# Optimization experiments

Measured on AMD Instinct MI355X. Metric: run time of the kernel, lower is better.

Reference implementation:

```python
import jax, jax.numpy as jnp
import numpy as np

BS = 1024
IN_DIM = 16 * 16      # final_dim[0]*final_dim[1]
HIDDEN = 3000
ITEM = 3              # item_number
STEPS = 30


def setup_inputs() -> dict:
    key = jax.random.key(0)
    ks = jax.random.split(key, 16)

    def xavier(k, shape):
        fan_in, fan_out = shape[1], shape[0]
        lim = np.sqrt(6.0 / (fan_in + fan_out))
        return jax.random.uniform(k, shape, jnp.float32, -lim, lim)

    return {
        "z": jax.random.normal(ks[0], (BS, 16, 16), jnp.float32),
        # join MLP: in->512->256->3000, ReLU after each
        "W1": xavier(ks[1], (512, IN_DIM)), "b1": jnp.zeros((512,), jnp.float32),
        "W2": xavier(ks[2], (256, 512)),    "b2": jnp.zeros((256,), jnp.float32),
        "W3": xavier(ks[3], (HIDDEN, 256)), "b3": jnp.zeros((HIDDEN,), jnp.float32),
        # GRUCell (torch layout: rows ordered r, z, n)
        "Wih": xavier(ks[4], (3 * HIDDEN, ITEM)),
        "bih": jnp.zeros((3 * HIDDEN,), jnp.float32),
        "Whh": xavier(ks[5], (3 * HIDDEN, HIDDEN)),
        "bhh": jnp.zeros((3 * HIDDEN,), jnp.float32),
        # output readout hidden -> item_number
        "Wo": xavier(ks[6], (ITEM, HIDDEN)), "bo": jnp.zeros((ITEM,), jnp.float32),
    }


def reference(z, W1, b1, W2, b2, W3, b3, Wih, bih, Whh, bhh, Wo, bo):
    bs = z.shape[0]
    zf = z.reshape(bs, -1)                                  # [bs, 256]
    h = jax.nn.relu(zf @ W1.T + b1)
    h = jax.nn.relu(h @ W2.T + b2)
    h = jax.nn.relu(h @ W3.T + b3)                          # [bs, 3000] initial hidden
    x0 = jnp.zeros((bs, ITEM), z.dtype)

    def step(carry, _):
        h, x = carry
        gi = x @ Wih.T + bih                                # [bs, 3H]
        gh = h @ Whh.T + bhh                                # [bs, 3H]
        i_r, i_z, i_n = jnp.split(gi, 3, axis=-1)
        h_r, h_z, h_n = jnp.split(gh, 3, axis=-1)
        r = jax.nn.sigmoid(i_r + h_r)
        u = jax.nn.sigmoid(i_z + h_z)
        n = jnp.tanh(i_n + r * h_n)
        h_new = (1.0 - u) * n + u * h
        x_new = h_new @ Wo.T + bo + x                       # residual waypoint add
        return (h_new, x_new), x_new

    (_, _), wp = jax.lax.scan(step, (h, x0), None, length=STEPS)
    return jnp.transpose(wp, (1, 0, 2))                      # [bs, STEPS, ITEM]
```

## Files before the change

kernel.cpp:

```cpp
#include <hip/hip_runtime.h>
#include <cstdint>
#include <cstddef>

#define HID 3000
#define HP  3072
#define NB  1024
#define BM  128
#define BN  64
#define KT  48

typedef _Float16 f16;
typedef _Float16 f16x8 __attribute__((ext_vector_type(8)));
typedef float    f32x4 __attribute__((ext_vector_type(4)));

__device__ __forceinline__ float sigf(float v)  { return 1.0f / (1.0f + __expf(-v)); }
__device__ __forceinline__ float tanhf_(float v){ return 2.0f / (1.0f + __expf(-2.0f * v)) - 1.0f; }

__device__ __forceinline__ void gload16(const void* g, void* l) {
    __builtin_amdgcn_global_load_lds((const __attribute__((address_space(1))) void*)g,
                                     (__attribute__((address_space(3))) void*)l, 16, 0, 0);
}

__global__ __launch_bounds__(256) void convert_whh(const float* __restrict__ whh,
                                                   f16* __restrict__ whh16)
{
    const int SLOTS = 3 * HP * (HP / 8);
    int t = blockIdx.x * 256 + threadIdx.x;
    if (t >= SLOTS) return;
    int c8 = (t % (HP / 8)) * 8;
    int rr = (t / (HP / 8)) % HP;
    int g  = t / ((HP / 8) * HP);
    f16x8 v;
#pragma unroll
    for (int i = 0; i < 8; ++i) v[i] = (f16)0.0f;
    if (rr < HID) {
        const float* src = whh + (size_t)(g * HID + rr) * HID;
#pragma unroll
        for (int i = 0; i < 8; ++i) {
            int c = c8 + i;
            if (c < HID) v[i] = (f16)src[c];
        }
    }
    *reinterpret_cast<f16x8*>(whh16 + ((size_t)g * HP + rr) * HP + c8) = v;
}

__global__ __launch_bounds__(256) void convert_w3(const float* __restrict__ w,
                                                  f16* __restrict__ w16)
{
    int t = blockIdx.x * 256 + threadIdx.x;
    if (t >= HP * 32) return;
    int rr = t >> 5, c8 = (t & 31) * 8;
    f16x8 v;
#pragma unroll
    for (int i = 0; i < 8; ++i)
        v[i] = (rr < HID) ? (f16)w[(size_t)rr * 256 + c8 + i] : (f16)0.0f;
    *reinterpret_cast<f16x8*>(w16 + (size_t)rr * 256 + c8) = v;
}

__global__ __launch_bounds__(256) void mlp_layer(const float* __restrict__ A, int K, int N, int ldo,
                                                 const float* __restrict__ W,
                                                 const float* __restrict__ bias,
                                                 float* __restrict__ outf, f16* __restrict__ outh)
{
    __shared__ float sA[4 * 512];
    const int b0 = blockIdx.x * 4;
    for (int idx = threadIdx.x; idx < 4 * K; idx += 256)
        sA[idx] = A[(size_t)b0 * K + idx];
    __syncthreads();
    for (int n = threadIdx.x; n < ldo; n += 256) {
        float acc[4] = {0.f, 0.f, 0.f, 0.f};
        if (n < N) {
            const float4* wr = reinterpret_cast<const float4*>(W + (size_t)n * K);
            for (int kk = 0; kk < (K >> 2); ++kk) {
                float4 w = wr[kk];
#pragma unroll
                for (int r = 0; r < 4; ++r) {
                    const float* ar = sA + r * K + kk * 4;
                    acc[r] += ar[0] * w.x + ar[1] * w.y + ar[2] * w.z + ar[3] * w.w;
                }
            }
            float bv = bias[n];
#pragma unroll
            for (int r = 0; r < 4; ++r) acc[r] = fmaxf(acc[r] + bv, 0.f);
        }
#pragma unroll
        for (int r = 0; r < 4; ++r) {
            outf[(size_t)(b0 + r) * ldo + n] = acc[r];
            if (outh) outh[(size_t)(b0 + r) * ldo + n] = (f16)acc[r];
        }
    }
}

__global__ __launch_bounds__(256, 2)
void mlp3_mfma(const f16* __restrict__ A, const f16* __restrict__ B,
               const float* __restrict__ bias,
               float* __restrict__ outf, f16* __restrict__ outh)
{
    __shared__ __align__(16) char smem[24576];
    char* sBm = smem + 16384;

    const int tid  = threadIdx.x;
    const int lane = tid & 63;
    const int wid  = tid >> 6;
    const int wm = wid >> 1, wn = wid & 1;
    const int l15 = lane & 15, lhi = lane >> 4;
    const int swz = (lane & 7) << 4;

    const int gm0 = blockIdx.y * BM, gn0 = blockIdx.x * BN;

    const f16* a_srcs[4]; char* a_ldst[4];
#pragma unroll
    for (int i = 0; i < 4; ++i) {
        const int d = (i * 4 + wid) * 64 + lane;
        const int r = d >> 3;
        const int c = (d & 7) ^ (r & 7);
        a_srcs[i] = A + (size_t)(gm0 + r) * 256 + c * 8;
        a_ldst[i] = smem + (i * 4 + wid) * 1024;
    }
    const f16* b_srcs[2]; char* b_ldst[2];
#pragma unroll
    for (int i = 0; i < 2; ++i) {
        const int d = (i * 4 + wid) * 64 + lane;
        const int rr = d >> 3;
        const int c = (d & 7) ^ (rr & 7);
        b_srcs[i] = B + (size_t)(gn0 + rr) * 256 + c * 8;
        b_ldst[i] = sBm + (i * 4 + wid) * 1024;
    }

    f32x4 acc[4][2];
#pragma unroll
    for (int m = 0; m < 4; ++m)
#pragma unroll
        for (int n = 0; n < 2; ++n) acc[m][n] = (f32x4){0.f, 0.f, 0.f, 0.f};

    for (int kt = 0; kt < 4; ++kt) {
        const int kg = kt * 64;
#pragma unroll
        for (int i = 0; i < 4; ++i) gload16(a_srcs[i] + kg, a_ldst[i]);
#pragma unroll
        for (int i = 0; i < 2; ++i) gload16(b_srcs[i] + kg, b_ldst[i]);
        __syncthreads();
#pragma unroll
        for (int kk = 0; kk < 2; ++kk) {
            const int ko = (kk * 64 + lhi * 16) ^ swz;
            f16x8 af[4], bf[2];
#pragma unroll
            for (int m = 0; m < 4; ++m)
                af[m] = *reinterpret_cast<const f16x8*>(smem + (wm * 64 + m * 16 + l15) * 128 + ko);
#pragma unroll
            for (int n = 0; n < 2; ++n)
                bf[n] = *reinterpret_cast<const f16x8*>(sBm + (wn * 32 + n * 16 + l15) * 128 + ko);
#pragma unroll
            for (int m = 0; m < 4; ++m)
#pragma unroll
                for (int n = 0; n < 2; ++n)
                    acc[m][n] = __builtin_amdgcn_mfma_f32_16x16x32_f16(af[m], bf[n], acc[m][n], 0, 0, 0);
        }
        __syncthreads();
    }

#pragma unroll
    for (int m = 0; m < 4; ++m) {
#pragma unroll
        for (int e = 0; e < 4; ++e) {
            const int b = gm0 + wm * 64 + m * 16 + lhi * 4 + e;
#pragma unroll
            for (int n = 0; n < 2; ++n) {
                const int j = gn0 + wn * 32 + n * 16 + l15;
                if (j < HID) {
                    float v = fmaxf(acc[m][n][e] + bias[j], 0.f);
                    outf[(size_t)b * HP + j] = v;
                    outh[(size_t)b * HP + j] = (f16)v;
                }
            }
        }
    }
}

__global__ __launch_bounds__(256, 2)
void gru_step(const f16* __restrict__ h16c, float* __restrict__ hf32,
              const f16* __restrict__ whh16,
              const float* __restrict__ xprev,
              const float* __restrict__ Wih, const float* __restrict__ bih,
              const float* __restrict__ bhh,
              f16* __restrict__ h16n)
{
    __shared__ __align__(16) char smem[69632];

    const int tid  = threadIdx.x;
    const int lane = tid & 63;
    const int wid  = tid >> 6;
    const int l15 = lane & 15, lhi = lane >> 4;
    const int swz = (lane & 7) << 4;

    const int id = blockIdx.x;
    const int xcd = id & 7, j0 = id >> 3;
    const int bn = xcd * 8 + (j0 >> 3), bm = j0 & 7;
    const int gm0 = bm * 128, gn0 = bn * 48;

    const f16* a_src[4];
#pragma unroll
    for (int i = 0; i < 4; ++i) {
        const int d = i * 256 + tid;
        const int r = d >> 3;
        const int c = (d & 7) ^ (r & 7);
        a_src[i] = h16c + (size_t)(gm0 + r) * HP + c * 8;
    }
    const f16* b_src[5];
#pragma unroll
    for (int i = 0; i < 5; ++i) {
        const int d = i * 256 + tid;
        const int g = d / 384;
        const int s = d - g * 384;
        const int rr = s >> 3;
        const int c = (s & 7) ^ (rr & 7);
        b_src[i] = whh16 + (size_t)g * HP * HP + (size_t)(gn0 + rr) * HP + c * 8;
    }

    f32x4 acc[3][2][3];
#pragma unroll
    for (int g = 0; g < 3; ++g)
#pragma unroll
        for (int m = 0; m < 2; ++m)
#pragma unroll
            for (int n = 0; n < 3; ++n) acc[g][m][n] = (f32x4){0.f, 0.f, 0.f, 0.f};

    {
#pragma unroll
        for (int i = 0; i < 4; ++i) gload16(a_src[i], smem + i * 4096 + wid * 1024);
#pragma unroll
        for (int i = 0; i < 4; ++i) gload16(b_src[i], smem + 16384 + i * 4096 + wid * 1024);
        if (tid < 128) gload16(b_src[4], smem + 32768 + wid * 1024);
    }
    __syncthreads();

    for (int kt = 0; kt < KT; ++kt) {
        char* cbuf = smem + (kt & 1) * 34816;
        if (kt + 1 < KT) {
            char* nbuf = smem + ((kt + 1) & 1) * 34816;
            const int kg = (kt + 1) * 64;
#pragma unroll
            for (int i = 0; i < 4; ++i) gload16(a_src[i] + kg, nbuf + i * 4096 + wid * 1024);
#pragma unroll
            for (int i = 0; i < 4; ++i) gload16(b_src[i] + kg, nbuf + 16384 + i * 4096 + wid * 1024);
            if (tid < 128) gload16(b_src[4] + kg, nbuf + 32768 + wid * 1024);
        }
#pragma unroll
        for (int kk = 0; kk < 2; ++kk) {
            const int ko = (kk * 64 + lhi * 16) ^ swz;
            f16x8 af[2], bf[3][3];
#pragma unroll
            for (int m = 0; m < 2; ++m)
                af[m] = *reinterpret_cast<const f16x8*>(cbuf + (wid * 32 + m * 16 + l15) * 128 + ko);
#pragma unroll
            for (int g = 0; g < 3; ++g)
#pragma unroll
                for (int n = 0; n < 3; ++n)
                    bf[g][n] = *reinterpret_cast<const f16x8*>(cbuf + 16384 + g * 6144 + (n * 16 + l15) * 128 + ko);
#pragma unroll
            for (int g = 0; g < 3; ++g)
#pragma unroll
                for (int m = 0; m < 2; ++m)
#pragma unroll
                    for (int n = 0; n < 3; ++n)
                        acc[g][m][n] = __builtin_amdgcn_mfma_f32_16x16x32_f16(af[m], bf[g][n], acc[g][m][n], 0, 0, 0);
        }
        __syncthreads();
    }

#pragma unroll
    for (int m = 0; m < 2; ++m) {
#pragma unroll
        for (int e = 0; e < 4; ++e) {
            const int b = gm0 + wid * 32 + m * 16 + lhi * 4 + e;
            const float x0 = xprev[b * 4 + 0], x1 = xprev[b * 4 + 1], x2 = xprev[b * 4 + 2];
#pragma unroll
            for (int n = 0; n < 3; ++n) {
                const int j = gn0 + n * 16 + l15;
                if (j < HID) {
                    float g0 = acc[0][m][n][e];
                    float g1 = acc[1][m][n][e];
                    float g2 = acc[2][m][n][e];
                    const float* wr = Wih + (size_t)j * 3;
                    const float* wz = Wih + (size_t)(HID + j) * 3;
                    const float* wn_ = Wih + (size_t)(2 * HID + j) * 3;
                    float gi0 = x0 * wr[0] + x1 * wr[1] + x2 * wr[2] + bih[j];
                    float gi1 = x0 * wz[0] + x1 * wz[1] + x2 * wz[2] + bih[HID + j];
                    float gi2 = x0 * wn_[0] + x1 * wn_[1] + x2 * wn_[2] + bih[2 * HID + j];
                    float r = sigf(gi0 + g0 + bhh[j]);
                    float u = sigf(gi1 + g1 + bhh[HID + j]);
                    float nn = tanhf_(gi2 + r * (g2 + bhh[2 * HID + j]));
                    float hp_ = hf32[(size_t)b * HP + j];
                    float hn = (1.f - u) * nn + u * hp_;
                    hf32[(size_t)b * HP + j] = hn;
                    h16n[(size_t)b * HP + j] = (f16)hn;
                }
            }
        }
    }
}

__global__ __launch_bounds__(256) void x_update(const f16* __restrict__ hn,
                                                const float* __restrict__ Wo,
                                                const float* __restrict__ bo,
                                                const float* __restrict__ xp,
                                                float* __restrict__ xn,
                                                float* __restrict__ out, int s)
{
    const int b = blockIdx.x, tid = threadIdx.x;
    float a0 = 0.f, a1 = 0.f, a2 = 0.f;
    for (int ch = tid; ch < 375; ch += 256) {
        const int k = ch * 8;
        f16x8 h8 = *reinterpret_cast<const f16x8*>(hn + (size_t)b * HP + k);
#pragma unroll
        for (int i = 0; i < 8; ++i) {
            float hv = (float)h8[i];
            a0 += hv * Wo[k + i];
            a1 += hv * Wo[HID + k + i];
            a2 += hv * Wo[2 * HID + k + i];
        }
    }
#pragma unroll
    for (int off = 32; off; off >>= 1) {
        a0 += __shfl_down(a0, off);
        a1 += __shfl_down(a1, off);
        a2 += __shfl_down(a2, off);
    }
    __shared__ float red[3][4];
    const int lane = tid & 63, w = tid >> 6;
    if (lane == 0) { red[0][w] = a0; red[1][w] = a1; red[2][w] = a2; }
    __syncthreads();
    if (tid < 3) {
        float sres = red[tid][0] + red[tid][1] + red[tid][2] + red[tid][3];
        float xv = sres + bo[tid] + xp[b * 4 + tid];
        xn[b * 4 + tid] = xv;
        out[((size_t)b * 30 + s) * 3 + tid] = xv;
    }
}

extern "C" void kernel_launch(void* const* d_in, const int* in_sizes, int n_in,
                              void* d_out, int out_size, void* d_ws, size_t ws_size,
                              hipStream_t stream)
{
    (void)in_sizes; (void)n_in; (void)out_size; (void)ws_size;
    const float* z   = (const float*)d_in[0];
    const float* W1  = (const float*)d_in[1];
    const float* b1  = (const float*)d_in[2];
    const float* W2  = (const float*)d_in[3];
    const float* b2  = (const float*)d_in[4];
    const float* W3  = (const float*)d_in[5];
    const float* b3  = (const float*)d_in[6];
    const float* Wih = (const float*)d_in[7];
    const float* bih = (const float*)d_in[8];
    const float* Whh = (const float*)d_in[9];
    const float* bhh = (const float*)d_in[10];
    const float* Wo  = (const float*)d_in[11];
    const float* bo  = (const float*)d_in[12];
    float* out = (float*)d_out;

    char* ws = (char*)d_ws;
    size_t off = 0;
    f16* whh16 = (f16*)(ws + off); off += (size_t)3 * HP * HP * 2;
    f16* h16[2];
    h16[0] = (f16*)(ws + off); off += (size_t)NB * HP * 2;
    h16[1] = (f16*)(ws + off); off += (size_t)NB * HP * 2;
    float* hf  = (float*)(ws + off); off += (size_t)NB * HP * 4;
    float* h1  = (float*)(ws + off); off += (size_t)NB * 512 * 4;
    float* h2  = (float*)(ws + off); off += (size_t)NB * 256 * 4;
    f16*   h2h = (f16*)(ws + off);   off += (size_t)NB * 256 * 2;
    f16*   w3f16 = (f16*)(ws + off); off += (size_t)HP * 256 * 2;
    float* xb  = (float*)(ws + off); off += (size_t)31 * NB * 4 * 4;

    hipMemsetAsync(h16[0], 0, (size_t)2 * NB * HP * 2, stream);
    hipMemsetAsync(xb, 0, (size_t)NB * 4 * 4, stream);

    {
        int slots = 3 * HP * (HP / 8);
        convert_whh<<<(slots + 255) / 256, 256, 0, stream>>>(Whh, whh16);
    }
    convert_w3<<<(HP * 32 + 255) / 256, 256, 0, stream>>>(W3, w3f16);

    mlp_layer<<<NB / 4, 256, 0, stream>>>(z,  256, 512, 512, W1, b1, h1, nullptr);
    mlp_layer<<<NB / 4, 256, 0, stream>>>(h1, 512, 256, 256, W2, b2, h2, h2h);
    mlp3_mfma<<<dim3(HP / BN, NB / BM), 256, 0, stream>>>(h2h, w3f16, b3, hf, h16[0]);

    for (int s = 1; s <= 30; ++s) {
        int cur = (s - 1) & 1, nxt = s & 1;
        gru_step<<<512, 256, 0, stream>>>(
            h16[cur], hf, whh16, xb + (size_t)(s - 1) * NB * 4,
            Wih, bih, bhh, h16[nxt]);
        x_update<<<NB, 256, 0, stream>>>(h16[nxt], Wo, bo,
            xb + (size_t)(s - 1) * NB * 4, xb + (size_t)s * NB * 4, out, s - 1);
    }
}
```

Measured before the change: 2.386 ms.

## Split K across warps in GRU step GEMM and vectorize weight conversion

The GRU step kernel now assigns each warp a 64-row M half and one of the two 32-wide K sub-slices per tile, instead of 32 rows over the full K tile. This doubles the MFMAs per A fragment load and cuts per-warp LDS reads of the shared B fragments, at the cost of 72 accumulator registers per lane and a two-pass shared-memory reduction with extra barriers before the epilogue. Only half the warps then run the gate epilogue. The weight conversion kernels also switch to float4 loads, which removes per-element bounds checks.

```diff
diff --git a/kernel.cpp b/kernel.cpp
--- a/kernel.cpp
+++ b/kernel.cpp
@@ -31,15 +31,15 @@
     int rr = (t / (HP / 8)) % HP;
     int g  = t / ((HP / 8) * HP);
     f16x8 v;
-#pragma unroll
-    for (int i = 0; i < 8; ++i) v[i] = (f16)0.0f;
-    if (rr < HID) {
-        const float* src = whh + (size_t)(g * HID + rr) * HID;
-#pragma unroll
-        for (int i = 0; i < 8; ++i) {
-            int c = c8 + i;
-            if (c < HID) v[i] = (f16)src[c];
-        }
+    if (rr < HID && c8 < HID) {
+        const float* src = whh + (size_t)(g * HID + rr) * HID + c8;
+        float4 lo = *reinterpret_cast<const float4*>(src);
+        float4 hi = *reinterpret_cast<const float4*>(src + 4);
+        v[0] = (f16)lo.x; v[1] = (f16)lo.y; v[2] = (f16)lo.z; v[3] = (f16)lo.w;
+        v[4] = (f16)hi.x; v[5] = (f16)hi.y; v[6] = (f16)hi.z; v[7] = (f16)hi.w;
+    } else {
+#pragma unroll
+        for (int i = 0; i < 8; ++i) v[i] = (f16)0.0f;
     }
     *reinterpret_cast<f16x8*>(whh16 + ((size_t)g * HP + rr) * HP + c8) = v;
 }
@@ -51,9 +51,16 @@
     if (t >= HP * 32) return;
     int rr = t >> 5, c8 = (t & 31) * 8;
     f16x8 v;
-#pragma unroll
-    for (int i = 0; i < 8; ++i)
-        v[i] = (rr < HID) ? (f16)w[(size_t)rr * 256 + c8 + i] : (f16)0.0f;
+    if (rr < HID) {
+        const float* src = w + (size_t)rr * 256 + c8;
+        float4 lo = *reinterpret_cast<const float4*>(src);
+        float4 hi = *reinterpret_cast<const float4*>(src + 4);
+        v[0] = (f16)lo.x; v[1] = (f16)lo.y; v[2] = (f16)lo.z; v[3] = (f16)lo.w;
+        v[4] = (f16)hi.x; v[5] = (f16)hi.y; v[6] = (f16)hi.z; v[7] = (f16)hi.w;
+    } else {
+#pragma unroll
+        for (int i = 0; i < 8; ++i) v[i] = (f16)0.0f;
+    }
     *reinterpret_cast<f16x8*>(w16 + (size_t)rr * 256 + c8) = v;
 }
 
@@ -190,6 +197,8 @@
     const int tid  = threadIdx.x;
     const int lane = tid & 63;
     const int wid  = tid >> 6;
+    const int wmh  = wid & 1;
+    const int ks   = wid >> 1;
     const int l15 = lane & 15, lhi = lane >> 4;
     const int swz = (lane & 7) << 4;
 
@@ -217,11 +226,11 @@
         b_src[i] = whh16 + (size_t)g * HP * HP + (size_t)(gn0 + rr) * HP + c * 8;
     }
 
-    f32x4 acc[3][2][3];
+    f32x4 acc[3][4][3];
 #pragma unroll
     for (int g = 0; g < 3; ++g)
 #pragma unroll
-        for (int m = 0; m < 2; ++m)
+        for (int m = 0; m < 4; ++m)
 #pragma unroll
             for (int n = 0; n < 3; ++n) acc[g][m][n] = (f32x4){0.f, 0.f, 0.f, 0.f};
 
@@ -245,22 +254,21 @@
             for (int i = 0; i < 4; ++i) gload16(b_src[i] + kg, nbuf + 16384 + i * 4096 + wid * 1024);
             if (tid < 128) gload16(b_src[4] + kg, nbuf + 32768 + wid * 1024);
         }
-#pragma unroll
-        for (int kk = 0; kk < 2; ++kk) {
-            const int ko = (kk * 64 + lhi * 16) ^ swz;
-            f16x8 af[2], bf[3][3];
-#pragma unroll
-            for (int m = 0; m < 2; ++m)
-                af[m] = *reinterpret_cast<const f16x8*>(cbuf + (wid * 32 + m * 16 + l15) * 128 + ko);
+        {
+            const int ko = (ks * 64 + lhi * 16) ^ swz;
+            f16x8 af[4], bf[3][3];
+#pragma unroll
+            for (int m = 0; m < 4; ++m)
+                af[m] = *reinterpret_cast<const f16x8*>(cbuf + (wmh * 64 + m * 16 + l15) * 128 + ko);
 #pragma unroll
             for (int g = 0; g < 3; ++g)
 #pragma unroll
                 for (int n = 0; n < 3; ++n)
-                    bf[g][n] = *reinterpret_cast<const f16x8*>(cbuf + 16384 + g * 6144 + (n * 16 + l15) * 128 + ko);
+                    bf[g][n] = *reinterpret_cast<const f16x8*>(cbuf + 16384 + (g * 48 + n * 16 + l15) * 128 + ko);
 #pragma unroll
             for (int g = 0; g < 3; ++g)
 #pragma unroll
-                for (int m = 0; m < 2; ++m)
+                for (int m = 0; m < 4; ++m)
 #pragma unroll
                     for (int n = 0; n < 3; ++n)
                         acc[g][m][n] = __builtin_amdgcn_mfma_f32_16x16x32_f16(af[m], bf[g][n], acc[g][m][n], 0, 0, 0);
@@ -268,11 +276,36 @@
         __syncthreads();
     }
 
-#pragma unroll
-    for (int m = 0; m < 2; ++m) {
+    f32x4* red = reinterpret_cast<f32x4*>(smem);
+#pragma unroll
+    for (int half = 0; half < 2; ++half) {
+        if (ks == 1) {
+#pragma unroll
+            for (int t = 0; t < 18; ++t) {
+                const int idx = half * 18 + t;
+                const int g = idx / 12, m = (idx / 3) % 4, n = idx % 3;
+                red[(wmh * 64 + lane) * 18 + t] = acc[g][m][n];
+            }
+        }
+        __syncthreads();
+        if (ks == 0) {
+#pragma unroll
+            for (int t = 0; t < 18; ++t) {
+                const int idx = half * 18 + t;
+                const int g = idx / 12, m = (idx / 3) % 4, n = idx % 3;
+                f32x4 v = red[(wmh * 64 + lane) * 18 + t];
+                acc[g][m][n] += v;
+            }
+        }
+        __syncthreads();
+    }
+    if (ks != 0) return;
+
+#pragma unroll
+    for (int m = 0; m < 4; ++m) {
 #pragma unroll
         for (int e = 0; e < 4; ++e) {
-            const int b = gm0 + wid * 32 + m * 16 + lhi * 4 + e;
+            const int b = gm0 + wmh * 64 + m * 16 + lhi * 4 + e;
             const float x0 = xprev[b * 4 + 0], x1 = xprev[b * 4 + 1], x2 = xprev[b * 4 + 2];
 #pragma unroll
             for (int n = 0; n < 3; ++n) {
```

Result: slower. 2.541 ms (+6.5%).

## Enlarge GRU step tiles to 256 rows with 12 waves and triple-buffered LDS pipeline

Applied to the files above, without the earlier changes.

The recurrent GEMM kernel now uses 768-thread blocks, each covering 256 batch rows by 48 hidden columns across all three gates. The grid drops to 256 blocks, so each Whh tile is fetched by half as many blocks. Global-to-LDS loads are triple-buffered with explicit vmcnt waits and raw barriers, and MFMA sections are raised in priority. The gate epilogue first stages accumulators through LDS, then does vectorized hf32 and f16 stores. The weight conversion kernels also switch to float4 reads. The cost is about 156 KB of LDS and one block per CU, so occupancy and latency hiding rest on 12 waves and the deeper pipeline.

```diff
diff --git a/kernel.cpp b/kernel.cpp
--- a/kernel.cpp
+++ b/kernel.cpp
@@ -8,6 +8,8 @@
 #define BM  128
 #define BN  64
 #define KT  48
+#define BUFSZ 51200
+#define PLANE 13312
 
 typedef _Float16 f16;
 typedef _Float16 f16x8 __attribute__((ext_vector_type(8)));
@@ -24,24 +26,37 @@
 __global__ __launch_bounds__(256) void convert_whh(const float* __restrict__ whh,
                                                    f16* __restrict__ whh16)
 {
-    const int SLOTS = 3 * HP * (HP / 8);
+    const int S32 = 3 * HP * (HP / 32);
     int t = blockIdx.x * 256 + threadIdx.x;
-    if (t >= SLOTS) return;
-    int c8 = (t % (HP / 8)) * 8;
-    int rr = (t / (HP / 8)) % HP;
-    int g  = t / ((HP / 8) * HP);
-    f16x8 v;
-#pragma unroll
-    for (int i = 0; i < 8; ++i) v[i] = (f16)0.0f;
-    if (rr < HID) {
-        const float* src = whh + (size_t)(g * HID + rr) * HID;
-#pragma unroll
-        for (int i = 0; i < 8; ++i) {
-            int c = c8 + i;
-            if (c < HID) v[i] = (f16)src[c];
-        }
-    }
-    *reinterpret_cast<f16x8*>(whh16 + ((size_t)g * HP + rr) * HP + c8) = v;
+    if (t >= S32) return;
+    const int c32 = (t % (HP / 32)) * 32;
+    const int rr  = (t / (HP / 32)) % HP;
+    const int g   = t / ((HP / 32) * HP);
+    f16* dst = whh16 + ((size_t)g * HP + rr) * HP + c32;
+    if (rr < HID && c32 + 32 <= HID) {
+        const float* src = whh + (size_t)(g * HID + rr) * HID + c32;
+#pragma unroll
+        for (int u = 0; u < 4; ++u) {
+            float4 lo = *reinterpret_cast<const float4*>(src + u * 8);
+            float4 hi = *reinterpret_cast<const float4*>(src + u * 8 + 4);
+            f16x8 v;
+            v[0] = (f16)lo.x; v[1] = (f16)lo.y; v[2] = (f16)lo.z; v[3] = (f16)lo.w;
+            v[4] = (f16)hi.x; v[5] = (f16)hi.y; v[6] = (f16)hi.z; v[7] = (f16)hi.w;
+            *reinterpret_cast<f16x8*>(dst + u * 8) = v;
+        }
+    } else {
+#pragma unroll
+        for (int u = 0; u < 4; ++u) {
+            f16x8 v;
+#pragma unroll
+            for (int k = 0; k < 8; ++k) {
+                const int cc = c32 + u * 8 + k;
+                v[k] = (rr < HID && cc < HID) ? (f16)whh[(size_t)(g * HID + rr) * HID + cc]
+                                              : (f16)0.0f;
+            }
+            *reinterpret_cast<f16x8*>(dst + u * 8) = v;
+        }
+    }
 }
 
 __global__ __launch_bounds__(256) void convert_w3(const float* __restrict__ w,
@@ -51,9 +66,16 @@
     if (t >= HP * 32) return;
     int rr = t >> 5, c8 = (t & 31) * 8;
     f16x8 v;
-#pragma unroll
-    for (int i = 0; i < 8; ++i)
-        v[i] = (rr < HID) ? (f16)w[(size_t)rr * 256 + c8 + i] : (f16)0.0f;
+    if (rr < HID) {
+        const float* src = w + (size_t)rr * 256 + c8;
+        float4 lo = *reinterpret_cast<const float4*>(src);
+        float4 hi = *reinterpret_cast<const float4*>(src + 4);
+        v[0] = (f16)lo.x; v[1] = (f16)lo.y; v[2] = (f16)lo.z; v[3] = (f16)lo.w;
+        v[4] = (f16)hi.x; v[5] = (f16)hi.y; v[6] = (f16)hi.z; v[7] = (f16)hi.w;
+    } else {
+#pragma unroll
+        for (int i = 0; i < 8; ++i) v[i] = (f16)0.0f;
+    }
     *reinterpret_cast<f16x8*>(w16 + (size_t)rr * 256 + c8) = v;
 }
 
@@ -177,7 +199,7 @@
     }
 }
 
-__global__ __launch_bounds__(256, 2)
+__global__ __launch_bounds__(768, 3)
 void gru_step(const f16* __restrict__ h16c, float* __restrict__ hf32,
               const f16* __restrict__ whh16,
               const float* __restrict__ xprev,
@@ -185,116 +207,156 @@
               const float* __restrict__ bhh,
               f16* __restrict__ h16n)
 {
-    __shared__ __align__(16) char smem[69632];
+    __shared__ __align__(16) char smem[159744];
 
     const int tid  = threadIdx.x;
     const int lane = tid & 63;
     const int wid  = tid >> 6;
+    const int wm   = wid & 3;
+    const int wn   = wid >> 2;
     const int l15 = lane & 15, lhi = lane >> 4;
     const int swz = (lane & 7) << 4;
 
     const int id = blockIdx.x;
-    const int xcd = id & 7, j0 = id >> 3;
-    const int bn = xcd * 8 + (j0 >> 3), bm = j0 & 7;
-    const int gm0 = bm * 128, gn0 = bn * 48;
-
-    const f16* a_src[4];
+    const int xcd = id & 7, local = id >> 3;
+    const int bn = xcd * 8 + (local >> 2), bm = local & 3;
+    const int gm0 = bm * 256, gn0 = bn * 48;
+
+    const f16* srcs[5];
 #pragma unroll
     for (int i = 0; i < 4; ++i) {
-        const int d = i * 256 + tid;
-        const int r = d >> 3;
-        const int c = (d & 7) ^ (r & 7);
-        a_src[i] = h16c + (size_t)(gm0 + r) * HP + c * 8;
-    }
-    const f16* b_src[5];
-#pragma unroll
-    for (int i = 0; i < 5; ++i) {
-        const int d = i * 256 + tid;
-        const int g = d / 384;
-        const int s = d - g * 384;
-        const int rr = s >> 3;
-        const int c = (s & 7) ^ (rr & 7);
-        b_src[i] = whh16 + (size_t)g * HP * HP + (size_t)(gn0 + rr) * HP + c * 8;
-    }
-
-    f32x4 acc[3][2][3];
-#pragma unroll
-    for (int g = 0; g < 3; ++g)
-#pragma unroll
-        for (int m = 0; m < 2; ++m)
-#pragma unroll
-            for (int n = 0; n < 3; ++n) acc[g][m][n] = (f32x4){0.f, 0.f, 0.f, 0.f};
-
+        const int s = i * 768 + tid;
+        if (s < 2048) {
+            const int r = s >> 3;
+            const int c = (s & 7) ^ (r & 7);
+            srcs[i] = h16c + (size_t)(gm0 + r) * HP + c * 8;
+        } else {
+            const int sb = s - 2048;
+            const int rr = sb >> 3;
+            const int g = rr / 48, jj = rr - g * 48;
+            const int c = (sb & 7) ^ (rr & 7);
+            srcs[i] = whh16 + (size_t)g * HP * HP + (size_t)(gn0 + jj) * HP + c * 8;
+        }
+    }
     {
-#pragma unroll
-        for (int i = 0; i < 4; ++i) gload16(a_src[i], smem + i * 4096 + wid * 1024);
-#pragma unroll
-        for (int i = 0; i < 4; ++i) gload16(b_src[i], smem + 16384 + i * 4096 + wid * 1024);
-        if (tid < 128) gload16(b_src[4], smem + 32768 + wid * 1024);
-    }
-    __syncthreads();
-
-    for (int kt = 0; kt < KT; ++kt) {
-        char* cbuf = smem + (kt & 1) * 34816;
-        if (kt + 1 < KT) {
-            char* nbuf = smem + ((kt + 1) & 1) * 34816;
-            const int kg = (kt + 1) * 64;
-#pragma unroll
-            for (int i = 0; i < 4; ++i) gload16(a_src[i] + kg, nbuf + i * 4096 + wid * 1024);
-#pragma unroll
-            for (int i = 0; i < 4; ++i) gload16(b_src[i] + kg, nbuf + 16384 + i * 4096 + wid * 1024);
-            if (tid < 128) gload16(b_src[4] + kg, nbuf + 32768 + wid * 1024);
-        }
+        const int sb = 1024 + tid;
+        const int rr = sb >> 3;
+        const int g = rr / 48, jj = rr - g * 48;
+        const int c = (sb & 7) ^ (rr & 7);
+        srcs[4] = whh16 + (size_t)g * HP * HP + (size_t)(gn0 + jj) * HP + c * 8;
+    }
+
+    f32x4 acc[4][3];
+#pragma unroll
+    for (int m = 0; m < 4; ++m)
+#pragma unroll
+        for (int n = 0; n < 3; ++n) acc[m][n] = (f32x4){0.f, 0.f, 0.f, 0.f};
+
+    auto STAGE = [&](int kt, char* bufc) {
+        const int ko = kt * 64;
+#pragma unroll
+        for (int i = 0; i < 4; ++i)
+            gload16(srcs[i] + ko, bufc + (i * 12 + wid) * 1024);
+        if (tid < 128) gload16(srcs[4] + ko, bufc + (48 + wid) * 1024);
+    };
+    auto COMPUTE = [&](const char* bufc) {
 #pragma unroll
         for (int kk = 0; kk < 2; ++kk) {
             const int ko = (kk * 64 + lhi * 16) ^ swz;
-            f16x8 af[2], bf[3][3];
-#pragma unroll
-            for (int m = 0; m < 2; ++m)
-                af[m] = *reinterpret_cast<const f16x8*>(cbuf + (wid * 32 + m * 16 + l15) * 128 + ko);
-#pragma unroll
-            for (int g = 0; g < 3; ++g)
+            f16x8 af[4], bf[3];
+#pragma unroll
+            for (int m = 0; m < 4; ++m)
+                af[m] = *reinterpret_cast<const f16x8*>(bufc + (wm * 64 + m * 16 + l15) * 128 + ko);
+#pragma unroll
+            for (int n = 0; n < 3; ++n)
+                bf[n] = *reinterpret_cast<const f16x8*>(bufc + 32768 + (wn * 48 + n * 16 + l15) * 128 + ko);
+            __builtin_amdgcn_s_setprio(1);
+#pragma unroll
+            for (int m = 0; m < 4; ++m)
 #pragma unroll
                 for (int n = 0; n < 3; ++n)
-                    bf[g][n] = *reinterpret_cast<const f16x8*>(cbuf + 16384 + g * 6144 + (n * 16 + l15) * 128 + ko);
-#pragma unroll
-            for (int g = 0; g < 3; ++g)
-#pragma unroll
-                for (int m = 0; m < 2; ++m)
-#pragma unroll
-                    for (int n = 0; n < 3; ++n)
-                        acc[g][m][n] = __builtin_amdgcn_mfma_f32_16x16x32_f16(af[m], bf[g][n], acc[g][m][n], 0, 0, 0);
-        }
-        __syncthreads();
-    }
-
-#pragma unroll
-    for (int m = 0; m < 2; ++m) {
-#pragma unroll
-        for (int e = 0; e < 4; ++e) {
-            const int b = gm0 + wid * 32 + m * 16 + lhi * 4 + e;
-            const float x0 = xprev[b * 4 + 0], x1 = xprev[b * 4 + 1], x2 = xprev[b * 4 + 2];
-#pragma unroll
-            for (int n = 0; n < 3; ++n) {
-                const int j = gn0 + n * 16 + l15;
-                if (j < HID) {
-                    float g0 = acc[0][m][n][e];
-                    float g1 = acc[1][m][n][e];
-                    float g2 = acc[2][m][n][e];
-                    const float* wr = Wih + (size_t)j * 3;
-                    const float* wz = Wih + (size_t)(HID + j) * 3;
-                    const float* wn_ = Wih + (size_t)(2 * HID + j) * 3;
-                    float gi0 = x0 * wr[0] + x1 * wr[1] + x2 * wr[2] + bih[j];
-                    float gi1 = x0 * wz[0] + x1 * wz[1] + x2 * wz[2] + bih[HID + j];
-                    float gi2 = x0 * wn_[0] + x1 * wn_[1] + x2 * wn_[2] + bih[2 * HID + j];
-                    float r = sigf(gi0 + g0 + bhh[j]);
-                    float u = sigf(gi1 + g1 + bhh[HID + j]);
-                    float nn = tanhf_(gi2 + r * (g2 + bhh[2 * HID + j]));
-                    float hp_ = hf32[(size_t)b * HP + j];
-                    float hn = (1.f - u) * nn + u * hp_;
-                    hf32[(size_t)b * HP + j] = hn;
-                    h16n[(size_t)b * HP + j] = (f16)hn;
-                }
+                    acc[m][n] = __builtin_amdgcn_mfma_f32_16x16x32_f16(af[m], bf[n], acc[m][n], 0, 0, 0);
+            __builtin_amdgcn_s_setprio(0);
+        }
+    };
+
+    STAGE(0, smem);
+    STAGE(1, smem + BUFSZ);
+
+    int cur = 0;
+    for (int t = 0; t < KT; ++t) {
+        if (t == KT - 1)      asm volatile("s_waitcnt vmcnt(0)" ::: "memory");
+        else if (wid < 2)     asm volatile("s_waitcnt vmcnt(5)" ::: "memory");
+        else                  asm volatile("s_waitcnt vmcnt(4)" ::: "memory");
+        __builtin_amdgcn_s_barrier();
+        __builtin_amdgcn_sched_barrier(0);
+        if (t + 2 < KT) {
+            int b2 = cur + 2; if (b2 >= 3) b2 -= 3;
+            STAGE(t + 2, smem + b2 * BUFSZ);
+        }
+        COMPUTE(smem + cur * BUFSZ);
+        ++cur; if (cur == 3) cur = 0;
+    }
+
+    __syncthreads();
+    float* planes = reinterpret_cast<float*>(smem);
+    {
+        float* myplane = planes + wn * PLANE;
+#pragma unroll
+        for (int m = 0; m < 4; ++m)
+#pragma unroll
+            for (int n = 0; n < 3; ++n)
+#pragma unroll
+                for (int e = 0; e < 4; ++e)
+                    myplane[(wm * 64 + m * 16 + lhi * 4 + e) * 52 + n * 16 + l15] = acc[m][n][e];
+    }
+    __syncthreads();
+
+#pragma unroll
+    for (int cc = 0; cc < 2; ++cc) {
+        const int c = tid + cc * 768;
+        const int row = c / 6;
+        const int coff = (c - row * 6) * 8;
+        const int b = gm0 + row;
+        const int jb = gn0 + coff;
+        if (jb >= HID) continue;
+        const float x0 = xprev[b * 4 + 0], x1 = xprev[b * 4 + 1], x2 = xprev[b * 4 + 2];
+        const int pb = row * 52 + coff;
+        const int nv = (jb + 8 <= HID) ? 8 : (HID - jb);
+        float hn[8];
+#pragma unroll
+        for (int i = 0; i < 8; ++i) {
+            if (i < nv) {
+                const int j = jb + i;
+                const float g0 = planes[pb + i];
+                const float g1 = planes[PLANE + pb + i];
+                const float g2 = planes[2 * PLANE + pb + i];
+                const float* w0 = Wih + (size_t)j * 3;
+                const float* w1 = Wih + (size_t)(HID + j) * 3;
+                const float* w2 = Wih + (size_t)(2 * HID + j) * 3;
+                const float gi0 = x0 * w0[0] + x1 * w0[1] + x2 * w0[2] + bih[j];
+                const float gi1 = x0 * w1[0] + x1 * w1[1] + x2 * w1[2] + bih[HID + j];
+                const float gi2 = x0 * w2[0] + x1 * w2[1] + x2 * w2[2] + bih[2 * HID + j];
+                const float r = sigf(gi0 + g0 + bhh[j]);
+                const float u = sigf(gi1 + g1 + bhh[HID + j]);
+                const float nn = tanhf_(gi2 + r * (g2 + bhh[2 * HID + j]));
+                const float hp_ = hf32[(size_t)b * HP + j];
+                hn[i] = (1.f - u) * nn + u * hp_;
+            }
+        }
+        if (nv == 8) {
+            f16x8 hv;
+#pragma unroll
+            for (int i = 0; i < 8; ++i) hv[i] = (f16)hn[i];
+            *reinterpret_cast<f16x8*>(h16n + (size_t)b * HP + jb) = hv;
+            float4 f0 = {hn[0], hn[1], hn[2], hn[3]};
+            float4 f1 = {hn[4], hn[5], hn[6], hn[7]};
+            *reinterpret_cast<float4*>(hf32 + (size_t)b * HP + jb) = f0;
+            *reinterpret_cast<float4*>(hf32 + (size_t)b * HP + jb + 4) = f1;
+        } else {
+            for (int i = 0; i < nv; ++i) {
+                hf32[(size_t)b * HP + jb + i] = hn[i];
+                h16n[(size_t)b * HP + jb + i] = (f16)hn[i];
             }
         }
     }
@@ -375,8 +437,8 @@
     hipMemsetAsync(xb, 0, (size_t)NB * 4 * 4, stream);
 
     {
-        int slots = 3 * HP * (HP / 8);
-        convert_whh<<<(slots + 255) / 256, 256, 0, stream>>>(Whh, whh16);
+        int s32 = 3 * HP * (HP / 32);
+        convert_whh<<<(s32 + 255) / 256, 256, 0, stream>>>(Whh, whh16);
     }
     convert_w3<<<(HP * 32 + 255) / 256, 256, 0, stream>>>(W3, w3f16);
 
@@ -386,7 +448,7 @@
 
     for (int s = 1; s <= 30; ++s) {
         int cur = (s - 1) & 1, nxt = s & 1;
-        gru_step<<<512, 256, 0, stream>>>(
+        gru_step<<<256, 768, 0, stream>>>(
             h16[cur], hf, whh16, xb + (size_t)(s - 1) * NB * 4,
             Wih, bih, bhh, h16[nxt]);
         x_update<<<NB, 256, 0, stream>>>(h16[nxt], Wo, bo,
```

Measured after the change: 2.182 ms. -8.5%, faster.
